# Kernel optimization log

Measured on AMD Instinct MI355X. Metric: run time of the kernel, lower is better.

The kernel has to match this reference:

```python
import jax, jax.numpy as jnp
import numpy as np

NUM_HEADS = 8
EMBED_DIM = 512


def _attention(q, k, v, mask=None):
    # q,k,v: [batch, heads, Lq, d] / [batch, heads, Lk, d]
    s = jnp.einsum('bhqd,bhkd->bhqk', q, k)
    if mask is not None:
        s = jnp.where(mask, jnp.asarray(-1000.0, s.dtype), s)
    p = jax.nn.softmax(s, axis=-1)
    return jnp.einsum('bhqk,bhkd->bhqd', p, v)


def _t_mask(T, H):
    # True where attention is DISALLOWED (query frame t_q < key frame t_k)
    tq = jnp.arange(T)[:, None]
    tk = jnp.arange(T)[None, :]
    blocked = tq < tk  # [T, T]
    m = jnp.repeat(jnp.repeat(blocked, H, axis=0), H, axis=1)  # [T*H, T*H]
    return m


def setup_inputs() -> dict:
    key = jax.random.key(0)
    ks = jax.random.split(key, 10)
    B, T, H, W, E = 4, 4, 28, 28, EMBED_DIM
    N = T * H * W
    s_in = (2.0 / (E + 3 * E)) ** 0.5  # xavier-ish
    s_sq = (1.0 / E) ** 0.5
    return {
        'x': jax.random.normal(ks[0], (B, N, E), dtype=jnp.float32),
        'in_proj_weight': jax.random.normal(ks[1], (3 * E, E), dtype=jnp.float32) * s_in,
        'in_proj_bias': jnp.zeros((3 * E,), dtype=jnp.float32),
        'out_proj_w': jax.random.normal(ks[2], (E, E), dtype=jnp.float32) * s_sq,
        'out_proj_b': jnp.zeros((E,), dtype=jnp.float32),
        'in_proj_weight_t': jax.random.normal(ks[3], (E, E), dtype=jnp.float32) * s_sq,
        'in_proj_bias_t': jnp.zeros((E,), dtype=jnp.float32),
        'out_proj_t_w': jax.random.normal(ks[4], (E, E), dtype=jnp.float32) * s_sq,
        'out_proj_t_b': jnp.zeros((E,), dtype=jnp.float32),
        'alpha': 0.0001 * jnp.ones((E,), dtype=jnp.float32),
        'H': 28,
        'W': 28,
    }


def reference(x, in_proj_weight, in_proj_bias, out_proj_w, out_proj_b,
              in_proj_weight_t, in_proj_bias_t, out_proj_t_w, out_proj_t_b,
              alpha, H, W):
    B, N, C = x.shape
    nh = NUM_HEADS
    hc = C // nh
    T = N // (H * W)
    scale = hc ** (-0.5)

    # ---- spatial (per-frame) attention: _forward_2d ----
    qkv = x @ in_proj_weight.T + in_proj_bias            # [B, N, 3C]
    qkv = qkv.reshape(B, T, H * W, 3, nh, hc)
    qkv = qkv.transpose(3, 0, 1, 4, 2, 5).reshape(3, B * T, nh, H * W, hc)
    q, k, v = qkv[0], qkv[1], qkv[2]
    o = _attention(q * scale, k, v)                       # [B*T, nh, HW, hc]
    xs = o.transpose(0, 2, 1, 3).reshape(B, N, C)
    xs = xs @ out_proj_w.T + out_proj_b

    ks = jax.lax.stop_gradient(k)                         # detached cache
    vs = jax.lax.stop_gradient(v)

    # ---- axial temporal attention ----
    q_t = (x @ in_proj_weight_t.T + in_proj_bias_t) * scale  # [B, N, C]
    q_t = q_t.reshape(B, T, H, W, nh, hc)
    q_th = q_t.transpose(0, 3, 4, 1, 2, 5).reshape(B * W, nh, T * H, hc)
    q_tw = q_t.transpose(0, 2, 4, 1, 3, 5).reshape(B * H, nh, T * W, hc)

    k6 = ks.reshape(B, T, nh, H, W, hc)
    v6 = vs.reshape(B, T, nh, H, W, hc)
    k_th = k6.transpose(0, 4, 2, 1, 3, 5).reshape(B * W, nh, T * H, hc)
    k_tw = k6.transpose(0, 3, 2, 1, 4, 5).reshape(B * H, nh, T * W, hc)
    v_th = v6.transpose(0, 4, 2, 1, 3, 5).reshape(B * W, nh, T * H, hc)
    v_tw = v6.transpose(0, 3, 2, 1, 4, 5).reshape(B * H, nh, T * W, hc)

    o_th = _attention(q_th, k_th, v_th, _t_mask(T, H))    # [B*W, nh, T*H, hc]
    o_tw = _attention(q_tw, k_tw, v_tw, _t_mask(T, W))    # [B*H, nh, T*W, hc]

    o_th = o_th.reshape(B, W, nh, T, H, hc).transpose(0, 3, 4, 1, 2, 5).reshape(B, N, C)
    o_tw = o_tw.reshape(B, H, nh, T, W, hc).transpose(0, 3, 1, 4, 2, 5).reshape(B, N, C)

    x_t = (o_th + o_tw) @ out_proj_t_w.T + out_proj_t_b
    return xs + alpha * x_t
```

## Files before the change

kernel.cpp:

```cpp
#include <hip/hip_runtime.h>
#include <stdint.h>

#define NN   3136
#define MM   12544
#define SCALE 0.125f
#define MASKED (-30000.0f)

typedef __attribute__((ext_vector_type(8))) unsigned short ushort8;
typedef __attribute__((ext_vector_type(8))) short short8;
typedef __attribute__((ext_vector_type(4))) float floatx4;

__device__ __forceinline__ float b2f(unsigned short u) {
    union { unsigned int i; float f; } x; x.i = ((unsigned int)u) << 16; return x.f;
}
__device__ __forceinline__ unsigned short f2b(float f) {
    union { float f; unsigned int i; } x; x.f = f;
    unsigned int r = x.i + 0x7fffu + ((x.i >> 16) & 1u);
    return (unsigned short)(r >> 16);
}
__device__ __forceinline__ void load8(const void* p, size_t e, int isf32, float o[8]) {
    if (isf32) {
        const float* f = (const float*)p + e;
        #pragma unroll
        for (int i = 0; i < 8; ++i) o[i] = f[i];
    } else {
        ushort8 u = *(const ushort8*)((const unsigned short*)p + e);
        #pragma unroll
        for (int i = 0; i < 8; ++i) o[i] = b2f(u[i]);
    }
}
__device__ __forceinline__ float load1(const void* p, int e, int isf32) {
    return isf32 ? ((const float*)p)[e] : b2f(((const unsigned short*)p)[e]);
}

__global__ void detect_dtype(const void* __restrict__ x, int* __restrict__ flagp)
{
    if (threadIdx.x == 0 && blockIdx.x == 0) {
        const unsigned short* u = (const unsigned short*)x;
        int c = 0;
        for (int i = 0; i < 512; ++i) {
            const float v = b2f(u[i]);
            if (!(v == v) || fabsf(v) > 1000.0f) ++c;
        }
        *flagp = (c >= 16) ? 1 : 0;
    }
}

__global__ __launch_bounds__(256) void convert_x(
    const int* __restrict__ flagp, const float* __restrict__ x,
    unsigned short* __restrict__ xb)
{
    if (!*flagp) return;
    const size_t i = ((size_t)blockIdx.x * 256 + threadIdx.x) * 8;
    const float4 a = *(const float4*)(x + i);
    const float4 b = *(const float4*)(x + i + 4);
    ushort8 o;
    o[0] = f2b(a.x); o[1] = f2b(a.y); o[2] = f2b(a.z); o[3] = f2b(a.w);
    o[4] = f2b(b.x); o[5] = f2b(b.y); o[6] = f2b(b.z); o[7] = f2b(b.w);
    *(ushort8*)(xb + i) = o;
}

__global__ __launch_bounds__(256) void convert_wp(
    const int* __restrict__ flagp, const void* __restrict__ Wi,
    const void* __restrict__ Wt, unsigned short* __restrict__ wp)
{
    const int isf32 = *flagp;
    const size_t e = ((size_t)blockIdx.x * 256 + threadIdx.x) * 8;
    const int row = (int)(e >> 9);
    const int col = (int)(e & 511);
    float v[8];
    if (row < 1536) load8(Wi, (size_t)row * 512 + col, isf32, v);
    else {
        load8(Wt, (size_t)(row - 1536) * 512 + col, isf32, v);
        #pragma unroll
        for (int u = 0; u < 8; ++u) v[u] *= SCALE;
    }
    ushort8 o;
    #pragma unroll
    for (int u = 0; u < 8; ++u) o[u] = f2b(v[u]);
    *(ushort8*)(wp + e) = o;
}

__global__ __launch_bounds__(256) void convert_wf(
    const int* __restrict__ flagp, const void* __restrict__ Wo,
    const void* __restrict__ Wto, const void* __restrict__ alp,
    unsigned short* __restrict__ qkv)
{
    const int isf32 = *flagp;
    const size_t e = ((size_t)blockIdx.x * 256 + threadIdx.x) * 8;
    const int row = (int)(e >> 10);
    const int k = (int)(e & 1023);
    float v[8];
    if (k < 512) load8(Wo, (size_t)row * 512 + k, isf32, v);
    else {
        const float a = load1(alp, row, isf32);
        load8(Wto, (size_t)row * 512 + (k - 512), isf32, v);
        #pragma unroll
        for (int u = 0; u < 8; ++u) v[u] *= a;
    }
    ushort8 o;
    #pragma unroll
    for (int u = 0; u < 8; ++u) o[u] = f2b(v[u]);
    *(ushort8*)(qkv + (size_t)row * 1536 + 512 + k) = o;
}

__global__ __launch_bounds__(256) void gemm_proj_mfma(
    const int* __restrict__ flagp, const void* __restrict__ x,
    const unsigned short* __restrict__ xb,
    const unsigned short* __restrict__ wp,
    const void* __restrict__ bi, const void* __restrict__ bt,
    unsigned short* __restrict__ qkv, unsigned short* __restrict__ qt)
{
    __shared__ unsigned short A_sh[128][40];
    __shared__ unsigned short B_sh[64][40];
    const int gid = blockIdx.x;
    const int mt = (gid >> 8) * 8 + (gid & 7);
    const int nt = (gid & 255) >> 3;
    if (mt >= 98) return;
    const int m0 = mt * 128, n0 = nt * 64;

    const int isf32 = *flagp;
    const unsigned short* A = isf32 ? xb : (const unsigned short*)x;
    const int tid = threadIdx.x, lane = tid & 63, wv = tid >> 6;
    const int lane15 = lane & 15, quad = lane >> 4;
    const int wm = wv >> 1, wn = wv & 1;

    const int ra = tid >> 1, ca = (tid & 1) * 16;
    const int rb = tid >> 2, cb = (tid & 3) * 8;
    const int nb = n0 + rb;

    floatx4 acc[4][2];
    #pragma unroll
    for (int i = 0; i < 4; ++i)
        #pragma unroll
        for (int j = 0; j < 2; ++j) acc[i][j] = (floatx4){0.f,0.f,0.f,0.f};

    for (int k0 = 0; k0 < 512; k0 += 32) {
        const unsigned short* ap = A + (size_t)(m0 + ra) * 512 + k0 + ca;
        *(ushort8*)&A_sh[ra][ca]     = *(const ushort8*)ap;
        *(ushort8*)&A_sh[ra][ca + 8] = *(const ushort8*)(ap + 8);
        *(ushort8*)&B_sh[rb][cb] = *(const ushort8*)(wp + (size_t)nb * 512 + k0 + cb);
        __syncthreads();

        short8 af[4], bf[2];
        #pragma unroll
        for (int i = 0; i < 4; ++i)
            af[i] = *(const short8*)&A_sh[wm * 64 + i * 16 + lane15][quad * 8];
        #pragma unroll
        for (int j = 0; j < 2; ++j)
            bf[j] = *(const short8*)&B_sh[wn * 32 + j * 16 + lane15][quad * 8];
        #pragma unroll
        for (int i = 0; i < 4; ++i)
            #pragma unroll
            for (int j = 0; j < 2; ++j)
                acc[i][j] = __builtin_amdgcn_mfma_f32_16x16x32_bf16(af[i], bf[j], acc[i][j], 0, 0, 0);
        __syncthreads();
    }

    #pragma unroll
    for (int j = 0; j < 2; ++j) {
        const int col = n0 + wn * 32 + j * 16 + lane15;
        float bias;
        unsigned short* dst;
        int stride;
        if (col < 1536) { bias = load1(bi, col, isf32); dst = qkv; stride = 1536; }
        else { bias = SCALE * load1(bt, col - 1536, isf32); dst = qt; stride = 512; }
        const int cofs = (col < 1536) ? col : (col - 1536);
        #pragma unroll
        for (int i = 0; i < 4; ++i)
            #pragma unroll
            for (int r = 0; r < 4; ++r) {
                const int m = m0 + wm * 64 + i * 16 + quad * 4 + r;
                dst[(size_t)m * stride + cofs] = f2b(acc[i][j][r] + bias);
            }
    }
}

__global__ __launch_bounds__(256) void gemm_final_mfma(
    const int* __restrict__ flagp,
    const unsigned short* __restrict__ qkv, const unsigned short* __restrict__ qt,
    const void* __restrict__ bo, const void* __restrict__ bto,
    const void* __restrict__ alp, void* __restrict__ outp)
{
    __shared__ unsigned short A_sh[128][40];
    __shared__ unsigned short B_sh[64][40];
    const int gid = blockIdx.x;
    const int mt = (gid >> 6) * 8 + (gid & 7);
    const int nt = (gid & 63) >> 3;
    if (mt >= 98) return;
    const int m0 = mt * 128, n0 = nt * 64;

    const int isf32 = *flagp;
    const int tid = threadIdx.x, lane = tid & 63, wv = tid >> 6;
    const int lane15 = lane & 15, quad = lane >> 4;
    const int wm = wv >> 1, wn = wv & 1;

    const int ra = tid >> 1, ca = (tid & 1) * 16;
    const int rb = tid >> 2, cb = (tid & 3) * 8;
    const int nb = n0 + rb;

    floatx4 acc[4][2];
    #pragma unroll
    for (int i = 0; i < 4; ++i)
        #pragma unroll
        for (int j = 0; j < 2; ++j) acc[i][j] = (floatx4){0.f,0.f,0.f,0.f};

    for (int k0 = 0; k0 < 1024; k0 += 32) {
        const int m = m0 + ra;
        const unsigned short* ap = (k0 < 512)
            ? qkv + (size_t)m * 1536 + k0 + ca
            : qt  + (size_t)m * 512  + (k0 - 512) + ca;
        *(ushort8*)&A_sh[ra][ca]     = *(const ushort8*)ap;
        *(ushort8*)&A_sh[ra][ca + 8] = *(const ushort8*)(ap + 8);
        *(ushort8*)&B_sh[rb][cb] =
            *(const ushort8*)(qkv + (size_t)nb * 1536 + 512 + k0 + cb);
        __syncthreads();

        short8 af[4], bf[2];
        #pragma unroll
        for (int i = 0; i < 4; ++i)
            af[i] = *(const short8*)&A_sh[wm * 64 + i * 16 + lane15][quad * 8];
        #pragma unroll
        for (int j = 0; j < 2; ++j)
            bf[j] = *(const short8*)&B_sh[wn * 32 + j * 16 + lane15][quad * 8];
        #pragma unroll
        for (int i = 0; i < 4; ++i)
            #pragma unroll
            for (int j = 0; j < 2; ++j)
                acc[i][j] = __builtin_amdgcn_mfma_f32_16x16x32_bf16(af[i], bf[j], acc[i][j], 0, 0, 0);
        __syncthreads();
    }

    #pragma unroll
    for (int j = 0; j < 2; ++j) {
        const int col = n0 + wn * 32 + j * 16 + lane15;
        const float bias = load1(bo, col, isf32) + load1(alp, col, isf32) * load1(bto, col, isf32);
        #pragma unroll
        for (int i = 0; i < 4; ++i)
            #pragma unroll
            for (int r = 0; r < 4; ++r) {
                const int m = m0 + wm * 64 + i * 16 + quad * 4 + r;
                const float val = acc[i][j][r] + bias;
                const size_t idx = (size_t)m * 512 + col;
                if (isf32) ((float*)outp)[idx] = val;
                else       ((unsigned short*)outp)[idx] = f2b(val);
            }
    }
}

__global__ __launch_bounds__(256) void attn_spatial_mfma(unsigned short* __restrict__ qkv)
{
    __shared__ unsigned short K_sh[64][72];
    __shared__ unsigned short VT_sh[64][72];
    __shared__ unsigned short P_sh[8][16][72];

    const int tid = threadIdx.x, lane = tid & 63, wv = tid >> 6;
    const int lane15 = lane & 15, quad = lane >> 4;

    const int gid = blockIdx.x;
    const int xcd = gid & 7, kk = gid >> 3;
    const int grp = xcd * 16 + kk / 7;
    const int qb  = kk % 7;
    const int head = grp & 7, bt = grp >> 3;

    const int t0 = qb * 8 + wv, t1 = t0 + 4;
    const bool act0 = (t0 < 49), act1 = (t1 < 49);
    const int q00 = act0 ? t0 * 16 : 0;
    const int q10 = act1 ? t1 * 16 : 0;
    const int frame0 = bt * 784;

    short8 q0_lo = {0,0,0,0,0,0,0,0}, q0_hi = {0,0,0,0,0,0,0,0};
    short8 q1_lo = {0,0,0,0,0,0,0,0}, q1_hi = {0,0,0,0,0,0,0,0};
    if (act0) {
        const unsigned short* qp = qkv + (size_t)(frame0 + q00 + lane15) * 1536 + head * 64 + quad * 8;
        q0_lo = *(const short8*)qp;
        q0_hi = *(const short8*)(qp + 32);
    }
    if (act1) {
        const unsigned short* qp = qkv + (size_t)(frame0 + q10 + lane15) * 1536 + head * 64 + quad * 8;
        q1_lo = *(const short8*)qp;
        q1_hi = *(const short8*)(qp + 32);
    }

    floatx4 accO0[4] = {{0.f,0.f,0.f,0.f},{0.f,0.f,0.f,0.f},{0.f,0.f,0.f,0.f},{0.f,0.f,0.f,0.f}};
    floatx4 accO1[4] = {{0.f,0.f,0.f,0.f},{0.f,0.f,0.f,0.f},{0.f,0.f,0.f,0.f},{0.f,0.f,0.f,0.f}};
    float ls0[4] = {0.f, 0.f, 0.f, 0.f};
    float ls1[4] = {0.f, 0.f, 0.f, 0.f};

    const int r_st = tid >> 2, c_st = (tid & 3) << 4;
    const int swzv = c_st;
    const int swzp = (lane15 >> 2) << 4;

    for (int kt = 0; kt < 13; ++kt) {
        __syncthreads();
        ushort8 k8a = {0,0,0,0,0,0,0,0}, k8b = {0,0,0,0,0,0,0,0};
        ushort8 v8a = {0,0,0,0,0,0,0,0}, v8b = {0,0,0,0,0,0,0,0};
        const int key = kt * 64 + r_st;
        if (key < 784) {
            const unsigned short* kp = qkv + (size_t)(frame0 + key) * 1536 + head * 64 + c_st;
            k8a = *(const ushort8*)(kp + 512);
            k8b = *(const ushort8*)(kp + 520);
            v8a = *(const ushort8*)(kp + 1024);
            v8b = *(const ushort8*)(kp + 1032);
        }
        *(ushort8*)&K_sh[r_st][c_st]     = k8a;
        *(ushort8*)&K_sh[r_st][c_st + 8] = k8b;
        #pragma unroll
        for (int u = 0; u < 8; ++u) {
            VT_sh[c_st + u][r_st ^ swzv]     = v8a[u];
            VT_sh[c_st + 8 + u][r_st ^ swzv] = v8b[u];
        }
        __syncthreads();

        floatx4 s0[4], s1[4];
        #pragma unroll
        for (int st = 0; st < 4; ++st) {
            const short8 kfl = *(const short8*)&K_sh[st * 16 + lane15][quad * 8];
            const short8 kfh = *(const short8*)&K_sh[st * 16 + lane15][32 + quad * 8];
            floatx4 a = {0.f,0.f,0.f,0.f};
            a = __builtin_amdgcn_mfma_f32_16x16x32_bf16(q0_lo, kfl, a, 0, 0, 0);
            a = __builtin_amdgcn_mfma_f32_16x16x32_bf16(q0_hi, kfh, a, 0, 0, 0);
            s0[st] = a;
            floatx4 b = {0.f,0.f,0.f,0.f};
            b = __builtin_amdgcn_mfma_f32_16x16x32_bf16(q1_lo, kfl, b, 0, 0, 0);
            b = __builtin_amdgcn_mfma_f32_16x16x32_bf16(q1_hi, kfh, b, 0, 0, 0);
            s1[st] = b;
        }

        const bool tail = (kt == 12);
        #pragma unroll
        for (int st = 0; st < 4; ++st)
            #pragma unroll
            for (int r = 0; r < 4; ++r) {
                const float v0 = (tail && st >= 1) ? MASKED : s0[st][r] * SCALE;
                const float p0 = __expf(v0);
                ls0[r] += p0;
                P_sh[wv][quad * 4 + r][(st * 16 + lane15) ^ (quad << 4)] = f2b(p0);
                const float v1 = (tail && st >= 1) ? MASKED : s1[st][r] * SCALE;
                const float p1 = __expf(v1);
                ls1[r] += p1;
                P_sh[wv + 4][quad * 4 + r][(st * 16 + lane15) ^ (quad << 4)] = f2b(p1);
            }

        #pragma unroll
        for (int kc = 0; kc < 2; ++kc) {
            const short8 pf0 = *(const short8*)&P_sh[wv][lane15][(kc * 32 + quad * 8) ^ swzp];
            const short8 pf1 = *(const short8*)&P_sh[wv + 4][lane15][(kc * 32 + quad * 8) ^ swzp];
            #pragma unroll
            for (int nt = 0; nt < 4; ++nt) {
                const short8 vf = *(const short8*)&VT_sh[nt * 16 + lane15][(kc * 32 + quad * 8) ^ (nt << 4)];
                accO0[nt] = __builtin_amdgcn_mfma_f32_16x16x32_bf16(pf0, vf, accO0[nt], 0, 0, 0);
                accO1[nt] = __builtin_amdgcn_mfma_f32_16x16x32_bf16(pf1, vf, accO1[nt], 0, 0, 0);
            }
        }
    }

    #pragma unroll
    for (int off = 1; off < 16; off <<= 1)
        #pragma unroll
        for (int r = 0; r < 4; ++r) {
            ls0[r] += __shfl_xor(ls0[r], off, 64);
            ls1[r] += __shfl_xor(ls1[r], off, 64);
        }

    if (act0) {
        #pragma unroll
        for (int nt = 0; nt < 4; ++nt)
            #pragma unroll
            for (int r = 0; r < 4; ++r) {
                const int qrow = q00 + quad * 4 + r;
                qkv[(size_t)(frame0 + qrow) * 1536 + head * 64 + nt * 16 + lane15]
                    = f2b(accO0[nt][r] / ls0[r]);
            }
    }
    if (act1) {
        #pragma unroll
        for (int nt = 0; nt < 4; ++nt)
            #pragma unroll
            for (int r = 0; r < 4; ++r) {
                const int qrow = q10 + quad * 4 + r;
                qkv[(size_t)(frame0 + qrow) * 1536 + head * 64 + nt * 16 + lane15]
                    = f2b(accO1[nt][r] / ls1[r]);
            }
    }
}

__global__ __launch_bounds__(256) void attn_axial(
    const unsigned short* __restrict__ qkv, const unsigned short* __restrict__ qtu,
    const unsigned short* __restrict__ oth, unsigned short* __restrict__ outp,
    const int pass)
{
    __shared__ unsigned short K_sh[112][72];
    __shared__ unsigned short VT_sh[64][136];
    __shared__ unsigned short P_sh[4][16][136];

    const int tid = threadIdx.x, lane = tid & 63, wv = tid >> 6;
    const int lane15 = lane & 15, quad = lane >> 4;
    const int b = blockIdx.x / 28, pos = blockIdx.x % 28;
    const int head = blockIdx.y;
    const int r_st = tid >> 3, c_st = (tid & 7) << 3;
    const int swzp = (lane15 >> 2) << 4;

    #pragma unroll
    for (int rnd = 0; rnd < 4; ++rnd) {
        const int j = rnd * 32 + r_st;
        if (j < 112) {
            const int tk = j / 28, rk = j % 28;
            const int n_k = tk * 784 + (pass == 0 ? rk * 28 + pos : pos * 28 + rk);
            const unsigned short* kp = qkv + (size_t)(b * NN + n_k) * 1536 + 512 + head * 64 + c_st;
            const ushort8 k8 = *(const ushort8*)kp;
            const ushort8 v8 = *(const ushort8*)(kp + 512);
            *(ushort8*)&K_sh[j][c_st] = k8;
            #pragma unroll
            for (int u = 0; u < 8; ++u) VT_sh[c_st + u][j ^ c_st] = v8[u];
        } else {
            #pragma unroll
            for (int u = 0; u < 8; ++u) VT_sh[c_st + u][j ^ c_st] = 0;
        }
    }
    __syncthreads();

    for (int tile = wv; tile < 7; tile += 4) {
        const int iq = tile * 16 + lane15;
        const int tq_q = iq / 28, rq = iq % 28;
        const int n_q = tq_q * 784 + (pass == 0 ? rq * 28 + pos : pos * 28 + rq);
        const size_t qaddr = (size_t)(b * NN + n_q) * 512 + head * 64;
        const short8 q_lo = *(const short8*)(qtu + qaddr + quad * 8);
        const short8 q_hi = *(const short8*)(qtu + qaddr + 32 + quad * 8);

        floatx4 s[7];
        #pragma unroll
        for (int st = 0; st < 7; ++st) {
            const short8 kfl = *(const short8*)&K_sh[st * 16 + lane15][quad * 8];
            const short8 kfh = *(const short8*)&K_sh[st * 16 + lane15][32 + quad * 8];
            floatx4 acc = {0.f,0.f,0.f,0.f};
            acc = __builtin_amdgcn_mfma_f32_16x16x32_bf16(q_lo, kfl, acc, 0, 0, 0);
            acc = __builtin_amdgcn_mfma_f32_16x16x32_bf16(q_hi, kfh, acc, 0, 0, 0);
            s[st] = acc;
        }

        int tq_row[4];
        #pragma unroll
        for (int r = 0; r < 4; ++r) tq_row[r] = (tile * 16 + quad * 4 + r) / 28;
        float l[4] = {0.f, 0.f, 0.f, 0.f};
        #pragma unroll
        for (int st = 0; st < 7; ++st) {
            const int tk = (st * 16 + lane15) / 28;
            #pragma unroll
            for (int r = 0; r < 4; ++r) {
                const float v = (tk <= tq_row[r]) ? s[st][r] : MASKED;
                const float p = __expf(v);
                s[st][r] = p;
                l[r] += p;
            }
        }
        #pragma unroll
        for (int off = 1; off < 16; off <<= 1)
            #pragma unroll
            for (int r = 0; r < 4; ++r)
                l[r] += __shfl_xor(l[r], off, 64);

        #pragma unroll
        for (int r = 0; r < 4; ++r) {
            const int row = quad * 4 + r;
            #pragma unroll
            for (int st = 0; st < 7; ++st)
                P_sh[wv][row][(st * 16 + lane15) ^ (quad << 4)] = f2b(s[st][r]);
            P_sh[wv][row][(112 + lane15) ^ (quad << 4)] = 0;
        }

        floatx4 accO[4] = {{0.f,0.f,0.f,0.f},{0.f,0.f,0.f,0.f},{0.f,0.f,0.f,0.f},{0.f,0.f,0.f,0.f}};
        #pragma unroll
        for (int kc = 0; kc < 4; ++kc) {
            const short8 pf = *(const short8*)&P_sh[wv][lane15][(kc * 32 + quad * 8) ^ swzp];
            #pragma unroll
            for (int nt = 0; nt < 4; ++nt) {
                const int row = nt * 16 + lane15;
                const short8 vf = *(const short8*)&VT_sh[row][(kc * 32 + quad * 8) ^ ((row >> 3) << 3)];
                accO[nt] = __builtin_amdgcn_mfma_f32_16x16x32_bf16(pf, vf, accO[nt], 0, 0, 0);
            }
        }

        #pragma unroll
        for (int r = 0; r < 4; ++r) {
            const int io = tile * 16 + quad * 4 + r;
            const int to = io / 28, ro = io % 28;
            const int n_o = to * 784 + (pass == 0 ? ro * 28 + pos : pos * 28 + ro);
            const size_t oaddr = (size_t)(b * NN + n_o) * 512 + head * 64;
            #pragma unroll
            for (int nt = 0; nt < 4; ++nt) {
                float o = accO[nt][r] / l[r];
                if (pass == 1) o += b2f(oth[oaddr + nt * 16 + lane15]);
                outp[oaddr + nt * 16 + lane15] = f2b(o);
            }
        }
    }
}

__global__ void fill_val(unsigned short* o, unsigned short v, int n) {
    const int i = blockIdx.x * 256 + threadIdx.x;
    if (i < n) o[i] = v;
}

extern "C" void kernel_launch(void* const* d_in, const int* in_sizes, int n_in,
                              void* d_out, int out_size, void* d_ws, size_t ws_size,
                              hipStream_t stream)
{
    const void* x   = d_in[0];
    const void* Wi  = d_in[1];
    const void* bi  = d_in[2];
    const void* Wo  = d_in[3];
    const void* bo  = d_in[4];
    const void* Wt  = d_in[5];
    const void* bt  = d_in[6];
    const void* Wto = d_in[7];
    const void* bto = d_in[8];
    const void* alp = d_in[9];

    const size_t QKV_ELEMS = (size_t)MM * 1536;
    const size_t QT_ELEMS  = (size_t)MM * 512;
    const size_t FLAG_OFF  = (QKV_ELEMS + QT_ELEMS) * 2;
    const size_t NEED      = FLAG_OFF + 256;

    if (ws_size < NEED) {
        fill_val<<<dim3((out_size + 255) / 256), dim3(256), 0, stream>>>(
            (unsigned short*)d_out, (unsigned short)0x3f80, out_size);
        return;
    }

    unsigned short* qkv = (unsigned short*)d_ws;
    unsigned short* qt  = qkv + QKV_ELEMS;
    int* flagp = (int*)((char*)d_ws + FLAG_OFF);
    unsigned short* oth = (unsigned short*)d_out;
    unsigned short* xb  = oth + (size_t)MM * 512;
    unsigned short* wp  = oth;

    dim3 blk(256);
    detect_dtype<<<dim3(1), dim3(64), 0, stream>>>(x, flagp);
    convert_x<<<dim3(MM * 512 / (256 * 8)), blk, 0, stream>>>(flagp, (const float*)x, xb);
    convert_wp<<<dim3(2048 * 512 / (256 * 8)), blk, 0, stream>>>(flagp, Wi, Wt, wp);
    gemm_proj_mfma<<<dim3(13 * 256), blk, 0, stream>>>(
        flagp, x, xb, wp, bi, bt, qkv, qt);
    attn_spatial_mfma<<<dim3(112 * 8), blk, 0, stream>>>(qkv);
    attn_axial<<<dim3(112, 8), blk, 0, stream>>>(qkv, qt, nullptr, oth, 0);
    attn_axial<<<dim3(112, 8), blk, 0, stream>>>(qkv, qt, oth, qt, 1);
    convert_wf<<<dim3(512 * 1024 / (256 * 8)), blk, 0, stream>>>(flagp, Wo, Wto, alp, qkv);
    gemm_final_mfma<<<dim3(13 * 64), blk, 0, stream>>>(
        flagp, qkv, qt, bo, bto, alp, d_out);
}
```

Baseline: 304.5 us.

## Prefetch next K/V tile into registers and fold softmax scale into K weights

```diff
diff --git a/kernel.cpp b/kernel.cpp
--- a/kernel.cpp
+++ b/kernel.cpp
@@ -4,6 +4,7 @@
 #define NN   3136
 #define MM   12544
 #define SCALE 0.125f
+#define KSCL  (0.125f * 1.44269504088896f)
 #define MASKED (-30000.0f)
 
 typedef __attribute__((ext_vector_type(8))) unsigned short ushort8;
@@ -70,10 +71,10 @@
     const int col = (int)(e & 511);
     float v[8];
     if (row < 1536) load8(Wi, (size_t)row * 512 + col, isf32, v);
-    else {
-        load8(Wt, (size_t)(row - 1536) * 512 + col, isf32, v);
-        #pragma unroll
-        for (int u = 0; u < 8; ++u) v[u] *= SCALE;
+    else            load8(Wt, (size_t)(row - 1536) * 512 + col, isf32, v);
+    if (row >= 512 && row < 1024) {
+        #pragma unroll
+        for (int u = 0; u < 8; ++u) v[u] *= KSCL;
     }
     ushort8 o;
     #pragma unroll
@@ -163,8 +164,12 @@
         float bias;
         unsigned short* dst;
         int stride;
-        if (col < 1536) { bias = load1(bi, col, isf32); dst = qkv; stride = 1536; }
-        else { bias = SCALE * load1(bt, col - 1536, isf32); dst = qt; stride = 512; }
+        if (col < 1536) {
+            bias = load1(bi, col, isf32);
+            if (col >= 512 && col < 1024) bias *= KSCL;
+            dst = qkv; stride = 1536;
+        }
+        else { bias = load1(bt, col - 1536, isf32); dst = qt; stride = 512; }
         const int cofs = (col < 1536) ? col : (col - 1536);
         #pragma unroll
         for (int i = 0; i < 4; ++i)
@@ -291,24 +296,30 @@
     const int swzv = c_st;
     const int swzp = (lane15 >> 2) << 4;
 
-    for (int kt = 0; kt < 13; ++kt) {
+    const unsigned short* kp0 = qkv + (size_t)(frame0 + r_st) * 1536 + head * 64 + c_st;
+    ushort8 rka = *(const ushort8*)(kp0 + 512);
+    ushort8 rkb = *(const ushort8*)(kp0 + 520);
+    ushort8 rva = *(const ushort8*)(kp0 + 1024);
+    ushort8 rvb = *(const ushort8*)(kp0 + 1032);
+
+    for (int kt = 0; kt < 12; ++kt) {
         __syncthreads();
-        ushort8 k8a = {0,0,0,0,0,0,0,0}, k8b = {0,0,0,0,0,0,0,0};
-        ushort8 v8a = {0,0,0,0,0,0,0,0}, v8b = {0,0,0,0,0,0,0,0};
-        const int key = kt * 64 + r_st;
-        if (key < 784) {
-            const unsigned short* kp = qkv + (size_t)(frame0 + key) * 1536 + head * 64 + c_st;
-            k8a = *(const ushort8*)(kp + 512);
-            k8b = *(const ushort8*)(kp + 520);
-            v8a = *(const ushort8*)(kp + 1024);
-            v8b = *(const ushort8*)(kp + 1032);
-        }
-        *(ushort8*)&K_sh[r_st][c_st]     = k8a;
-        *(ushort8*)&K_sh[r_st][c_st + 8] = k8b;
+        *(ushort8*)&K_sh[r_st][c_st]     = rka;
+        *(ushort8*)&K_sh[r_st][c_st + 8] = rkb;
         #pragma unroll
         for (int u = 0; u < 8; ++u) {
-            VT_sh[c_st + u][r_st ^ swzv]     = v8a[u];
-            VT_sh[c_st + 8 + u][r_st ^ swzv] = v8b[u];
+            VT_sh[c_st + u][r_st ^ swzv]     = rva[u];
+            VT_sh[c_st + 8 + u][r_st ^ swzv] = rvb[u];
+        }
+        ushort8 nka = {0,0,0,0,0,0,0,0}, nkb = {0,0,0,0,0,0,0,0};
+        ushort8 nva = {0,0,0,0,0,0,0,0}, nvb = {0,0,0,0,0,0,0,0};
+        const int nkey = (kt + 1) * 64 + r_st;
+        if (nkey < 784) {
+            const unsigned short* kp = qkv + (size_t)(frame0 + nkey) * 1536 + head * 64 + c_st;
+            nka = *(const ushort8*)(kp + 512);
+            nkb = *(const ushort8*)(kp + 520);
+            nva = *(const ushort8*)(kp + 1024);
+            nvb = *(const ushort8*)(kp + 1032);
         }
         __syncthreads();
 
@@ -327,21 +338,66 @@
             s1[st] = b;
         }
 
-        const bool tail = (kt == 12);
         #pragma unroll
         for (int st = 0; st < 4; ++st)
             #pragma unroll
             for (int r = 0; r < 4; ++r) {
-                const float v0 = (tail && st >= 1) ? MASKED : s0[st][r] * SCALE;
-                const float p0 = __expf(v0);
+                const float p0 = exp2f(s0[st][r]);
                 ls0[r] += p0;
                 P_sh[wv][quad * 4 + r][(st * 16 + lane15) ^ (quad << 4)] = f2b(p0);
-                const float v1 = (tail && st >= 1) ? MASKED : s1[st][r] * SCALE;
-                const float p1 = __expf(v1);
+                const float p1 = exp2f(s1[st][r]);
                 ls1[r] += p1;
                 P_sh[wv + 4][quad * 4 + r][(st * 16 + lane15) ^ (quad << 4)] = f2b(p1);
             }
 
+        #pragma unroll
+        for (int kc = 0; kc < 2; ++kc) {
+            const short8 pf0 = *(const short8*)&P_sh[wv][lane15][(kc * 32 + quad * 8) ^ swzp];
+            const short8 pf1 = *(const short8*)&P_sh[wv + 4][lane15][(kc * 32 + quad * 8) ^ swzp];
+            #pragma unroll
+            for (int nt = 0; nt < 4; ++nt) {
+                const short8 vf = *(const short8*)&VT_sh[nt * 16 + lane15][(kc * 32 + quad * 8) ^ (nt << 4)];
+                accO0[nt] = __builtin_amdgcn_mfma_f32_16x16x32_bf16(pf0, vf, accO0[nt], 0, 0, 0);
+                accO1[nt] = __builtin_amdgcn_mfma_f32_16x16x32_bf16(pf1, vf, accO1[nt], 0, 0, 0);
+            }
+        }
+        rka = nka; rkb = nkb; rva = nva; rvb = nvb;
+    }
+
+    __syncthreads();
+    *(ushort8*)&K_sh[r_st][c_st]     = rka;
+    *(ushort8*)&K_sh[r_st][c_st + 8] = rkb;
+    #pragma unroll
+    for (int u = 0; u < 8; ++u) {
+        VT_sh[c_st + u][r_st ^ swzv]     = rva[u];
+        VT_sh[c_st + 8 + u][r_st ^ swzv] = rvb[u];
+    }
+    __syncthreads();
+    {
+        const short8 kfl = *(const short8*)&K_sh[lane15][quad * 8];
+        const short8 kfh = *(const short8*)&K_sh[lane15][32 + quad * 8];
+        floatx4 a = {0.f,0.f,0.f,0.f};
+        a = __builtin_amdgcn_mfma_f32_16x16x32_bf16(q0_lo, kfl, a, 0, 0, 0);
+        a = __builtin_amdgcn_mfma_f32_16x16x32_bf16(q0_hi, kfh, a, 0, 0, 0);
+        floatx4 b = {0.f,0.f,0.f,0.f};
+        b = __builtin_amdgcn_mfma_f32_16x16x32_bf16(q1_lo, kfl, b, 0, 0, 0);
+        b = __builtin_amdgcn_mfma_f32_16x16x32_bf16(q1_hi, kfh, b, 0, 0, 0);
+        #pragma unroll
+        for (int r = 0; r < 4; ++r) {
+            const float p0 = exp2f(a[r]);
+            ls0[r] += p0;
+            P_sh[wv][quad * 4 + r][lane15 ^ (quad << 4)] = f2b(p0);
+            const float p1 = exp2f(b[r]);
+            ls1[r] += p1;
+            P_sh[wv + 4][quad * 4 + r][lane15 ^ (quad << 4)] = f2b(p1);
+        }
+        #pragma unroll
+        for (int st = 1; st < 4; ++st)
+            #pragma unroll
+            for (int r = 0; r < 4; ++r) {
+                P_sh[wv][quad * 4 + r][(st * 16 + lane15) ^ (quad << 4)] = 0;
+                P_sh[wv + 4][quad * 4 + r][(st * 16 + lane15) ^ (quad << 4)] = 0;
+            }
         #pragma unroll
         for (int kc = 0; kc < 2; ++kc) {
             const short8 pf0 = *(const short8*)&P_sh[wv][lane15][(kc * 32 + quad * 8) ^ swzp];
@@ -449,7 +505,7 @@
             #pragma unroll
             for (int r = 0; r < 4; ++r) {
                 const float v = (tk <= tq_row[r]) ? s[st][r] : MASKED;
-                const float p = __expf(v);
+                const float p = exp2f(v);
                 s[st][r] = p;
                 l[r] += p;
             }
```

After: 305.6 us. About the same (+0.4%).
